# Optimization experiments

Hardware: AMD Instinct MI355X
Metric: run time of the kernel (lower is better)

Reference implementation:

```python
import jax, jax.numpy as jnp
import numpy as np
import math

B, M, C, H = 4, 2048, 512, 8
DQK = C // 4 // H  # 16 per-head query/key dim


def setup_inputs() -> dict:
    key = jax.random.key(0)
    ks = jax.random.split(key, 8)
    s = 0.02
    return {
        "x": jax.random.normal(ks[0], (B, M, C), dtype=jnp.float32),
        "mask": jax.random.randint(ks[1], (B, M), 0, 2, dtype=jnp.int32),
        "Wq": jax.random.normal(ks[2], (C, C // 4), dtype=jnp.float32) * s,
        "bq": jnp.zeros((C // 4,), dtype=jnp.float32),
        "Wk": jax.random.normal(ks[3], (C, C // 4), dtype=jnp.float32) * s,
        "bk": jnp.zeros((C // 4,), dtype=jnp.float32),
        "Wv": jax.random.normal(ks[4], (C, C), dtype=jnp.float32) * s,
        "bv": jnp.zeros((C,), dtype=jnp.float32),
        "gamma": jnp.ones((1,), dtype=jnp.float32),
    }


def reference(x, mask, Wq, bq, Wk, bk, Wv, bv, gamma):
    b, m, c = x.shape
    # projections, split heads: q/k -> (B, H, M, DQK), v -> (B, H, M, C//H)
    q = (x @ Wq + bq).reshape(b, m, H, -1).transpose(0, 2, 1, 3)
    k = (x @ Wk + bk).reshape(b, m, H, -1).transpose(0, 2, 1, 3)
    v = (x @ Wv + bv).reshape(b, m, H, -1).transpose(0, 2, 1, 3)
    scale = 1.0 / math.sqrt(q.shape[-1])
    scores = jnp.einsum('bhmd,bhnd->bhmn', q, k) * scale
    beta = jax.nn.softmax(jax.nn.relu(scores), axis=-1)  # act='relu' pre-softmax
    # att_drop = 0.0 -> identity
    mf = mask.astype(x.dtype)[:, None, None, :]  # (B,1,1,M)
    beta = beta * mf
    beta = beta / (beta.sum(-1, keepdims=True) + 1e-12)
    o = gamma * jnp.einsum('bhmn,bhnd->bhmd', beta, v)  # (B,H,M,C//H)
    return o.transpose(0, 2, 1, 3).reshape(b, m, c)
```

## Files before the change

kernel.cpp:

```cpp
#include <hip/hip_runtime.h>
#include <hip/hip_bf16.h>

#define MSEQ 2048

typedef __attribute__((ext_vector_type(8))) short short8;
typedef __attribute__((ext_vector_type(4))) short short4v;
typedef __attribute__((ext_vector_type(4))) float f32x4;

static __device__ __forceinline__ short bf16b(float f) {
    __hip_bfloat16 h = __float2bfloat16(f);
    return *reinterpret_cast<short*>(&h);
}

static __device__ __forceinline__ void gl_lds16(const void* g, void* l) {
    __builtin_amdgcn_global_load_lds(
        (const __attribute__((address_space(1))) unsigned int*)g,
        (__attribute__((address_space(3))) unsigned int*)l, 16, 0, 0);
}

__global__ __launch_bounds__(256) void xcvt_kernel(
    const float* __restrict__ x, unsigned short* __restrict__ xb)
{
    const size_t i = ((size_t)blockIdx.x * 256 + threadIdx.x) * 8;
    const float4 a = *(const float4*)(x + i);
    const float4 b = *(const float4*)(x + i + 4);
    short8 o;
    o[0]=bf16b(a.x); o[1]=bf16b(a.y); o[2]=bf16b(a.z); o[3]=bf16b(a.w);
    o[4]=bf16b(b.x); o[5]=bf16b(b.y); o[6]=bf16b(b.z); o[7]=bf16b(b.w);
    *(short8*)(xb + i) = o;
}

__global__ __launch_bounds__(256) void wtrans_kernel(
    const float* __restrict__ Wq, const float* __restrict__ Wk,
    const float* __restrict__ Wv, unsigned short* __restrict__ WT)
{
    const int nt = blockIdx.x;
    const int kt = blockIdx.y;
    const int t  = threadIdx.x;
    const int k0 = kt*64;

    const float* W; int ld, n0;
    if (nt < 2)      { W = Wq; ld = 128; n0 = nt*64; }
    else if (nt < 4) { W = Wk; ld = 128; n0 = (nt-2)*64; }
    else             { W = Wv; ld = 512; n0 = (nt-4)*64; }

    __shared__ unsigned short Ts[64*72];

    #pragma unroll
    for (int s = 0; s < 4; ++s) {
        const int lin = s*256 + t;
        const int krow = lin >> 4, ng = lin & 15;
        const float4 v = *(const float4*)(W + (size_t)(k0+krow)*ld + n0 + ng*4);
        Ts[(ng*4+0)*72 + krow] = (unsigned short)bf16b(v.x);
        Ts[(ng*4+1)*72 + krow] = (unsigned short)bf16b(v.y);
        Ts[(ng*4+2)*72 + krow] = (unsigned short)bf16b(v.z);
        Ts[(ng*4+3)*72 + krow] = (unsigned short)bf16b(v.w);
    }
    __syncthreads();
    #pragma unroll
    for (int s = 0; s < 2; ++s) {
        const int lin = s*256 + t;
        const int nrow = lin >> 3, kg = lin & 7;
        *(short8*)(WT + (size_t)(nt*64 + nrow)*512 + k0 + kg*8) = *(const short8*)&Ts[nrow*72 + kg*8];
    }
}

__global__ __launch_bounds__(256, 2) void proj_mfma(
    const unsigned short* __restrict__ xb, const unsigned short* __restrict__ WT,
    const float* __restrict__ bq, const float* __restrict__ bk, const float* __restrict__ bv,
    unsigned short* __restrict__ Qb, unsigned short* __restrict__ Kb, unsigned short* __restrict__ Vt)
{
    const int nt = blockIdx.x;
    const int r0 = blockIdx.y * 128;
    const int n0 = nt * 128;
    const int t = threadIdx.x, w = t >> 6, lane = t & 63, l15 = lane & 15, quad = lane >> 4;
    const int qh = w >> 1, chh = w & 1;

    __shared__ short smem[128*136];
    short* As = smem;
    short* Bs = smem + 128*32;

    f32x4 acc[4][4];
    #pragma unroll
    for (int i = 0; i < 4; ++i)
        #pragma unroll
        for (int j = 0; j < 4; ++j) acc[i][j] = {0.f,0.f,0.f,0.f};

    const int arow = lane >> 2, akg = lane & 3;

    for (int kk = 0; kk < 512; kk += 32) {
        #pragma unroll
        for (int s = 0; s < 2; ++s) {
            const int row = w*32 + s*16 + arow;
            gl_lds16(xb + (size_t)(r0+row)*512 + kk + akg*8, As + (w*32 + s*16)*32);
            gl_lds16(WT + (size_t)(n0+row)*512 + kk + akg*8, Bs + (w*32 + s*16)*32);
        }
        __syncthreads();
        short8 Af[4], Bf[4];
        #pragma unroll
        for (int i = 0; i < 4; ++i) Af[i] = *(const short8*)&As[(qh*64 + i*16 + l15)*32 + quad*8];
        #pragma unroll
        for (int j = 0; j < 4; ++j) Bf[j] = *(const short8*)&Bs[(chh*64 + j*16 + l15)*32 + quad*8];
        #pragma unroll
        for (int i = 0; i < 4; ++i)
            #pragma unroll
            for (int j = 0; j < 4; ++j)
                acc[i][j] = __builtin_amdgcn_mfma_f32_16x16x32_bf16(Af[i], Bf[j], acc[i][j], 0, 0, 0);
        __syncthreads();
    }

    const float* bias = (nt == 0) ? bq : (nt == 1) ? bk : (bv + (nt-2)*128);
    float bj[4];
    #pragma unroll
    for (int j = 0; j < 4; ++j) bj[j] = bias[chh*64 + j*16 + l15];

    short* Ts = smem;
    if (nt < 2) {
        #pragma unroll
        for (int i = 0; i < 4; ++i)
            #pragma unroll
            for (int j = 0; j < 4; ++j)
                #pragma unroll
                for (int r = 0; r < 4; ++r)
                    Ts[(qh*64 + i*16 + quad*4 + r)*136 + chh*64 + j*16 + l15] =
                        bf16b(acc[i][j][r] + bj[j]);
    } else {
        #pragma unroll
        for (int i = 0; i < 4; ++i)
            #pragma unroll
            for (int j = 0; j < 4; ++j)
                #pragma unroll
                for (int r = 0; r < 4; ++r)
                    Ts[(chh*64 + j*16 + l15)*136 + qh*64 + i*16 + quad*4 + r] =
                        bf16b(acc[i][j][r] + bj[j]);
    }
    __syncthreads();

    if (nt < 2) {
        unsigned short* Out = (nt == 0) ? Qb : Kb;
        #pragma unroll
        for (int s = 0; s < 8; ++s) {
            const int lin = s*256 + t, row = lin >> 4, seg = lin & 15;
            *(short8*)(Out + (size_t)(r0+row)*128 + seg*8) = *(const short8*)&Ts[row*136 + seg*8];
        }
    } else {
        const int b = r0 >> 11, key0 = r0 & 2047, chBase = (nt-2)*128;
        #pragma unroll
        for (int s = 0; s < 8; ++s) {
            const int lin = s*256 + t, row = lin >> 4, seg = lin & 15;
            *(short8*)(Vt + ((size_t)(b*512 + chBase + row))*MSEQ + key0 + seg*8) =
                *(const short8*)&Ts[row*136 + seg*8];
        }
    }
}

__global__ __launch_bounds__(256, 4) void attn_mfma(
    const unsigned short* __restrict__ Qb, const unsigned short* __restrict__ Kb,
    const unsigned short* __restrict__ Vt, const int* __restrict__ mask,
    const float* __restrict__ gamma, float* __restrict__ out)
{
    const int bh = blockIdx.x;
    const int b  = bh >> 3, h = bh & 7;
    const int m0 = blockIdx.y * 64;
    const int t  = threadIdx.x;
    const int wave = t >> 6, lane = t & 63, l15 = lane & 15, quad = lane >> 4;

    __shared__ short Ks[64*24];
    __shared__ short Qs[64*24];
    __shared__ short VtS[64*72];
    __shared__ short Ws[64*72];
    __shared__ float msk[64];
    __shared__ float wsl[4*64];
    __shared__ float wsums[64];

    if (t < 64) {
        short8 z = {0,0,0,0,0,0,0,0};
        *(short8*)&Ks[t*24 + 16] = z;
        *(short8*)&Qs[t*24 + 16] = z;
    }
    if (t < 128) {
        const int row = t >> 1, half = t & 1;
        *(short8*)&Qs[row*24 + half*8] =
            *(const short8*)(Qb + (size_t)(b*MSEQ + m0 + row)*128 + h*16 + half*8);
    }
    __syncthreads();

    const int kso = (quad < 2) ? quad*8 : 16;
    short8 qfrag[4];
    #pragma unroll
    for (int c = 0; c < 4; ++c)
        qfrag[c] = *(const short8*)&Qs[(c*16 + l15)*24 + kso];

    f32x4 acc[2][2] = {{{0.f,0.f,0.f,0.f},{0.f,0.f,0.f,0.f}},
                       {{0.f,0.f,0.f,0.f},{0.f,0.f,0.f,0.f}}};
    float wsum_acc[4] = {0.f,0.f,0.f,0.f};
    const int qh = wave >> 1, chh = wave & 1;

    for (int kt = 0; kt < 32; ++kt) {
        const int kn0 = kt*64;
        if (t < 128) {
            const int key = t >> 1, half = t & 1;
            *(short8*)&Ks[key*24 + half*8] =
                *(const short8*)(Kb + (size_t)(b*MSEQ + kn0 + key)*128 + h*16 + half*8);
        }
        #pragma unroll
        for (int i = 0; i < 2; ++i) {
            const int idx = i*256 + t;
            const int kg = idx & 7, ch = idx >> 3;
            *(short8*)&VtS[ch*72 + kg*8] =
                *(const short8*)(Vt + ((size_t)(b*512 + h*64 + ch))*MSEQ + kn0 + kg*8);
        }
        if (t < 64) msk[t] = (float)mask[b*MSEQ + kn0 + t];
        __syncthreads();

        const short8 kfrag = *(const short8*)&Ks[(wave*16 + l15)*24 + kso];
        const float4 mk4 = *(const float4*)&msk[wave*16 + quad*4];
        #pragma unroll
        for (int c = 0; c < 4; ++c) {
            f32x4 s = {0.f,0.f,0.f,0.f};
            s = __builtin_amdgcn_mfma_f32_16x16x32_bf16(kfrag, qfrag[c], s, 0, 0, 0);
            float w0 = mk4.x * __expf(fmaxf(0.25f*s[0], 0.f));
            float w1 = mk4.y * __expf(fmaxf(0.25f*s[1], 0.f));
            float w2 = mk4.z * __expf(fmaxf(0.25f*s[2], 0.f));
            float w3 = mk4.w * __expf(fmaxf(0.25f*s[3], 0.f));
            short4v ws4;
            ws4[0]=bf16b(w0); ws4[1]=bf16b(w1); ws4[2]=bf16b(w2); ws4[3]=bf16b(w3);
            *(short4v*)&Ws[(c*16 + l15)*72 + wave*16 + quad*4] = ws4;
            float tsum = (w0 + w1) + (w2 + w3);
            tsum += __shfl_xor(tsum, 16, 64);
            tsum += __shfl_xor(tsum, 32, 64);
            wsum_acc[c] += tsum;
        }
        __syncthreads();

        short8 Af[2][2], Bf[2][2];
        #pragma unroll
        for (int si = 0; si < 2; ++si)
            #pragma unroll
            for (int kh = 0; kh < 2; ++kh)
                Af[si][kh] = *(const short8*)&Ws[((qh*2+si)*16 + l15)*72 + kh*32 + quad*8];
        #pragma unroll
        for (int ci = 0; ci < 2; ++ci)
            #pragma unroll
            for (int kh = 0; kh < 2; ++kh)
                Bf[ci][kh] = *(const short8*)&VtS[((chh*2+ci)*16 + l15)*72 + kh*32 + quad*8];
        #pragma unroll
        for (int si = 0; si < 2; ++si)
            #pragma unroll
            for (int ci = 0; ci < 2; ++ci)
                #pragma unroll
                for (int kh = 0; kh < 2; ++kh)
                    acc[si][ci] = __builtin_amdgcn_mfma_f32_16x16x32_bf16(
                        Af[si][kh], Bf[ci][kh], acc[si][ci], 0, 0, 0);
        __syncthreads();
    }

    if (quad == 0) {
        #pragma unroll
        for (int c = 0; c < 4; ++c) wsl[wave*64 + c*16 + l15] = wsum_acc[c];
    }
    __syncthreads();
    if (t < 64) wsums[t] = (wsl[t] + wsl[64+t]) + (wsl[128+t] + wsl[192+t]);
    __syncthreads();

    const float g = gamma[0];
    #pragma unroll
    for (int si = 0; si < 2; ++si) {
        #pragma unroll
        for (int r = 0; r < 4; ++r) {
            const int row = qh*32 + si*16 + quad*4 + r;
            const float inv = g / fmaxf(wsums[row], 1e-20f);
            #pragma unroll
            for (int ci = 0; ci < 2; ++ci) {
                const int col = chh*32 + ci*16 + l15;
                out[(size_t)(b*MSEQ + m0 + row)*512 + h*64 + col] = acc[si][ci][r] * inv;
            }
        }
    }
}

extern "C" void kernel_launch(void* const* d_in, const int* in_sizes, int n_in,
                              void* d_out, int out_size, void* d_ws, size_t ws_size,
                              hipStream_t stream) {
    const float* x     = (const float*)d_in[0];
    const int*   mask  = (const int*)  d_in[1];
    const float* Wq    = (const float*)d_in[2];
    const float* bq    = (const float*)d_in[3];
    const float* Wk    = (const float*)d_in[4];
    const float* bk    = (const float*)d_in[5];
    const float* Wv    = (const float*)d_in[6];
    const float* bv    = (const float*)d_in[7];
    const float* gamma = (const float*)d_in[8];
    float* outp = (float*)d_out;

    unsigned short* xb = (unsigned short*)d_ws;
    unsigned short* WT = xb + (size_t)8192*512;
    unsigned short* Qb = WT + (size_t)768*512;
    unsigned short* Kb = Qb + (size_t)8192*128;
    unsigned short* Vt = Kb + (size_t)8192*128;

    xcvt_kernel<<<2048, 256, 0, stream>>>(x, xb);
    wtrans_kernel<<<dim3(12, 8), 256, 0, stream>>>(Wq, Wk, Wv, WT);
    proj_mfma<<<dim3(6, 64), 256, 0, stream>>>(xb, WT, bq, bk, bv, Qb, Kb, Vt);
    attn_mfma<<<dim3(32, 32), 256, 0, stream>>>(Qb, Kb, Vt, mask, gamma, outp);
}
```

Baseline: 168.2 us.

## Halve attention query tile, fold log2e scale into K, use raw exp2

The attention kernel now processes 32 query rows per block instead of 64, doubling the grid and raising the occupancy hint to 8 blocks per CU. The softmax scale times log2(e) is folded into the K projection output, so the inner loop can use a raw v_exp_f32 without a multiply. The per-iteration cross-lane row-sum shuffles are deferred to a single reduction after the loop. In exchange, K and V tiles are reloaded twice as often across blocks, and the scale is now applied before the bf16 rounding of K, which slightly changes precision.

Result: no change. 167.1 us (-0.7%).

```diff
diff --git a/kernel.cpp b/kernel.cpp
--- a/kernel.cpp
+++ b/kernel.cpp
@@ -10,6 +10,12 @@
 static __device__ __forceinline__ short bf16b(float f) {
     __hip_bfloat16 h = __float2bfloat16(f);
     return *reinterpret_cast<short*>(&h);
+}
+
+static __device__ __forceinline__ float fast_exp2(float x) {
+    float r;
+    asm("v_exp_f32 %0, %1" : "=v"(r) : "v"(x));
+    return r;
 }
 
 static __device__ __forceinline__ void gl_lds16(const void* g, void* l) {
@@ -110,6 +116,7 @@
     }
 
     const float* bias = (nt == 0) ? bq : (nt == 1) ? bk : (bv + (nt-2)*128);
+    const float kscale = (nt == 1) ? 0.36067376022224085f : 1.0f;
     float bj[4];
     #pragma unroll
     for (int j = 0; j < 4; ++j) bj[j] = bias[chh*64 + j*16 + l15];
@@ -123,7 +130,7 @@
                 #pragma unroll
                 for (int r = 0; r < 4; ++r)
                     Ts[(qh*64 + i*16 + quad*4 + r)*136 + chh*64 + j*16 + l15] =
-                        bf16b(acc[i][j][r] + bj[j]);
+                        bf16b((acc[i][j][r] + bj[j]) * kscale);
     } else {
         #pragma unroll
         for (int i = 0; i < 4; ++i)
@@ -154,31 +161,31 @@
     }
 }
 
-__global__ __launch_bounds__(256, 4) void attn_mfma(
+__global__ __launch_bounds__(256, 8) void attn_mfma(
     const unsigned short* __restrict__ Qb, const unsigned short* __restrict__ Kb,
     const unsigned short* __restrict__ Vt, const int* __restrict__ mask,
     const float* __restrict__ gamma, float* __restrict__ out)
 {
     const int bh = blockIdx.x;
     const int b  = bh >> 3, h = bh & 7;
-    const int m0 = blockIdx.y * 64;
+    const int m0 = blockIdx.y * 32;
     const int t  = threadIdx.x;
     const int wave = t >> 6, lane = t & 63, l15 = lane & 15, quad = lane >> 4;
 
     __shared__ short Ks[64*24];
-    __shared__ short Qs[64*24];
+    __shared__ short Qs[32*24];
     __shared__ short VtS[64*72];
-    __shared__ short Ws[64*72];
+    __shared__ short Ws[32*72];
     __shared__ float msk[64];
-    __shared__ float wsl[4*64];
-    __shared__ float wsums[64];
-
+    __shared__ float wsl[4*32];
+    __shared__ float wsums[32];
+
+    {
+        short8 z = {0,0,0,0,0,0,0,0};
+        if (t < 64) *(short8*)&Ks[t*24 + 16] = z;
+        if (t < 32) *(short8*)&Qs[t*24 + 16] = z;
+    }
     if (t < 64) {
-        short8 z = {0,0,0,0,0,0,0,0};
-        *(short8*)&Ks[t*24 + 16] = z;
-        *(short8*)&Qs[t*24 + 16] = z;
-    }
-    if (t < 128) {
         const int row = t >> 1, half = t & 1;
         *(short8*)&Qs[row*24 + half*8] =
             *(const short8*)(Qb + (size_t)(b*MSEQ + m0 + row)*128 + h*16 + half*8);
@@ -186,14 +193,13 @@
     __syncthreads();
 
     const int kso = (quad < 2) ? quad*8 : 16;
-    short8 qfrag[4];
-    #pragma unroll
-    for (int c = 0; c < 4; ++c)
+    short8 qfrag[2];
+    #pragma unroll
+    for (int c = 0; c < 2; ++c)
         qfrag[c] = *(const short8*)&Qs[(c*16 + l15)*24 + kso];
 
-    f32x4 acc[2][2] = {{{0.f,0.f,0.f,0.f},{0.f,0.f,0.f,0.f}},
-                       {{0.f,0.f,0.f,0.f},{0.f,0.f,0.f,0.f}}};
-    float wsum_acc[4] = {0.f,0.f,0.f,0.f};
+    f32x4 acc[2] = {{0.f,0.f,0.f,0.f},{0.f,0.f,0.f,0.f}};
+    float wsum_acc[2] = {0.f,0.f};
     const int qh = wave >> 1, chh = wave & 1;
 
     for (int kt = 0; kt < 32; ++kt) {
@@ -216,65 +222,58 @@
         const short8 kfrag = *(const short8*)&Ks[(wave*16 + l15)*24 + kso];
         const float4 mk4 = *(const float4*)&msk[wave*16 + quad*4];
         #pragma unroll
-        for (int c = 0; c < 4; ++c) {
+        for (int c = 0; c < 2; ++c) {
             f32x4 s = {0.f,0.f,0.f,0.f};
             s = __builtin_amdgcn_mfma_f32_16x16x32_bf16(kfrag, qfrag[c], s, 0, 0, 0);
-            float w0 = mk4.x * __expf(fmaxf(0.25f*s[0], 0.f));
-            float w1 = mk4.y * __expf(fmaxf(0.25f*s[1], 0.f));
-            float w2 = mk4.z * __expf(fmaxf(0.25f*s[2], 0.f));
-            float w3 = mk4.w * __expf(fmaxf(0.25f*s[3], 0.f));
+            float w0 = mk4.x * fast_exp2(fmaxf(s[0], 0.f));
+            float w1 = mk4.y * fast_exp2(fmaxf(s[1], 0.f));
+            float w2 = mk4.z * fast_exp2(fmaxf(s[2], 0.f));
+            float w3 = mk4.w * fast_exp2(fmaxf(s[3], 0.f));
             short4v ws4;
             ws4[0]=bf16b(w0); ws4[1]=bf16b(w1); ws4[2]=bf16b(w2); ws4[3]=bf16b(w3);
             *(short4v*)&Ws[(c*16 + l15)*72 + wave*16 + quad*4] = ws4;
-            float tsum = (w0 + w1) + (w2 + w3);
-            tsum += __shfl_xor(tsum, 16, 64);
-            tsum += __shfl_xor(tsum, 32, 64);
-            wsum_acc[c] += tsum;
-        }
-        __syncthreads();
-
-        short8 Af[2][2], Bf[2][2];
-        #pragma unroll
-        for (int si = 0; si < 2; ++si)
-            #pragma unroll
-            for (int kh = 0; kh < 2; ++kh)
-                Af[si][kh] = *(const short8*)&Ws[((qh*2+si)*16 + l15)*72 + kh*32 + quad*8];
+            wsum_acc[c] += (w0 + w1) + (w2 + w3);
+        }
+        __syncthreads();
+
+        short8 Af[2], Bf[2][2];
+        #pragma unroll
+        for (int kh = 0; kh < 2; ++kh)
+            Af[kh] = *(const short8*)&Ws[(qh*16 + l15)*72 + kh*32 + quad*8];
         #pragma unroll
         for (int ci = 0; ci < 2; ++ci)
             #pragma unroll
             for (int kh = 0; kh < 2; ++kh)
                 Bf[ci][kh] = *(const short8*)&VtS[((chh*2+ci)*16 + l15)*72 + kh*32 + quad*8];
         #pragma unroll
-        for (int si = 0; si < 2; ++si)
-            #pragma unroll
-            for (int ci = 0; ci < 2; ++ci)
-                #pragma unroll
-                for (int kh = 0; kh < 2; ++kh)
-                    acc[si][ci] = __builtin_amdgcn_mfma_f32_16x16x32_bf16(
-                        Af[si][kh], Bf[ci][kh], acc[si][ci], 0, 0, 0);
-        __syncthreads();
-    }
-
-    if (quad == 0) {
-        #pragma unroll
-        for (int c = 0; c < 4; ++c) wsl[wave*64 + c*16 + l15] = wsum_acc[c];
-    }
-    __syncthreads();
-    if (t < 64) wsums[t] = (wsl[t] + wsl[64+t]) + (wsl[128+t] + wsl[192+t]);
+        for (int ci = 0; ci < 2; ++ci)
+            #pragma unroll
+            for (int kh = 0; kh < 2; ++kh)
+                acc[ci] = __builtin_amdgcn_mfma_f32_16x16x32_bf16(
+                    Af[kh], Bf[ci][kh], acc[ci], 0, 0, 0);
+        __syncthreads();
+    }
+
+    #pragma unroll
+    for (int c = 0; c < 2; ++c) {
+        float r = wsum_acc[c];
+        r += __shfl_xor(r, 16, 64);
+        r += __shfl_xor(r, 32, 64);
+        if (quad == 0) wsl[wave*32 + c*16 + l15] = r;
+    }
+    __syncthreads();
+    if (t < 32) wsums[t] = (wsl[t] + wsl[32+t]) + (wsl[64+t] + wsl[96+t]);
     __syncthreads();
 
     const float g = gamma[0];
     #pragma unroll
-    for (int si = 0; si < 2; ++si) {
-        #pragma unroll
-        for (int r = 0; r < 4; ++r) {
-            const int row = qh*32 + si*16 + quad*4 + r;
-            const float inv = g / fmaxf(wsums[row], 1e-20f);
-            #pragma unroll
-            for (int ci = 0; ci < 2; ++ci) {
-                const int col = chh*32 + ci*16 + l15;
-                out[(size_t)(b*MSEQ + m0 + row)*512 + h*64 + col] = acc[si][ci][r] * inv;
-            }
+    for (int r = 0; r < 4; ++r) {
+        const int row = qh*16 + quad*4 + r;
+        const float inv = g / fmaxf(wsums[row], 1e-20f);
+        #pragma unroll
+        for (int ci = 0; ci < 2; ++ci) {
+            const int col = chh*32 + ci*16 + l15;
+            out[(size_t)(b*MSEQ + m0 + row)*512 + h*64 + col] = acc[ci][r] * inv;
         }
     }
 }
@@ -302,5 +301,5 @@
     xcvt_kernel<<<2048, 256, 0, stream>>>(x, xb);
     wtrans_kernel<<<dim3(12, 8), 256, 0, stream>>>(Wq, Wk, Wv, WT);
     proj_mfma<<<dim3(6, 64), 256, 0, stream>>>(xb, WT, bq, bk, bv, Qb, Kb, Vt);
-    attn_mfma<<<dim3(32, 32), 256, 0, stream>>>(Qb, Kb, Vt, mask, gamma, outp);
-}
+    attn_mfma<<<dim3(32, 64), 256, 0, stream>>>(Qb, Kb, Vt, mask, gamma, outp);
+}
```

## Split keys across waves in attention kernel, drop LDS staging, fold scale into K

Applied to the files above, without the earlier changes.

The attention kernel now gives each wave a quarter of the key sequence. Each wave loads K, V and mask fragments straight from global memory into registers and uses 16x16x16 bf16 MFMAs that keep P in registers, so the per-tile LDS round trip and the two barriers per key tile go away. The 1/sqrt(d)*log2(e) factor is folded into K during the projection, so the softmax uses a raw v_exp_f32 (exp2). The cost is a final cross-wave reduction of the output accumulators through LDS. Global loads are now uncoalesced, small and not shared across waves, and each thread holds more accumulator registers.

New measurement: 187.9 us. 11.7% more time.

```diff
diff --git a/kernel.cpp b/kernel.cpp
--- a/kernel.cpp
+++ b/kernel.cpp
@@ -10,6 +10,16 @@
 static __device__ __forceinline__ short bf16b(float f) {
     __hip_bfloat16 h = __float2bfloat16(f);
     return *reinterpret_cast<short*>(&h);
+}
+
+static __device__ __forceinline__ float fast_exp2(float x) {
+    float r;
+    asm("v_exp_f32 %0, %1" : "=v"(r) : "v"(x));
+    return r;
+}
+
+static __device__ __forceinline__ f32x4 mfma16(short4v a, short4v b, f32x4 c) {
+    return __builtin_amdgcn_mfma_f32_16x16x16bf16_1k(a, b, c, 0, 0, 0);
 }
 
 static __device__ __forceinline__ void gl_lds16(const void* g, void* l) {
@@ -110,6 +120,7 @@
     }
 
     const float* bias = (nt == 0) ? bq : (nt == 1) ? bk : (bv + (nt-2)*128);
+    const float kscale = (nt == 1) ? 0.36067376022224085f : 1.0f;
     float bj[4];
     #pragma unroll
     for (int j = 0; j < 4; ++j) bj[j] = bias[chh*64 + j*16 + l15];
@@ -123,7 +134,7 @@
                 #pragma unroll
                 for (int r = 0; r < 4; ++r)
                     Ts[(qh*64 + i*16 + quad*4 + r)*136 + chh*64 + j*16 + l15] =
-                        bf16b(acc[i][j][r] + bj[j]);
+                        bf16b((acc[i][j][r] + bj[j]) * kscale);
     } else {
         #pragma unroll
         for (int i = 0; i < 4; ++i)
@@ -163,119 +174,101 @@
     const int b  = bh >> 3, h = bh & 7;
     const int m0 = blockIdx.y * 64;
     const int t  = threadIdx.x;
-    const int wave = t >> 6, lane = t & 63, l15 = lane & 15, quad = lane >> 4;
-
-    __shared__ short Ks[64*24];
-    __shared__ short Qs[64*24];
-    __shared__ short VtS[64*72];
-    __shared__ short Ws[64*72];
-    __shared__ float msk[64];
+    const int w = t >> 6, lane = t & 63, l15 = lane & 15, quad = lane >> 4;
+
+    short4v qf[4];
+    #pragma unroll
+    for (int c = 0; c < 4; ++c)
+        qf[c] = *(const short4v*)(Qb + (size_t)(b*MSEQ + m0 + c*16 + l15)*128 + h*16 + quad*4);
+
+    f32x4 O[4][4];
+    #pragma unroll
+    for (int c = 0; c < 4; ++c)
+        #pragma unroll
+        for (int v = 0; v < 4; ++v) O[c][v] = {0.f,0.f,0.f,0.f};
+    float ws_acc[4] = {0.f,0.f,0.f,0.f};
+
+    const unsigned short* Kp = Kb + (size_t)(b*MSEQ + w*512 + l15)*128 + h*16 + quad*4;
+    const unsigned short* Vp = Vt + ((size_t)(b*512 + h*64 + l15))*MSEQ + w*512 + quad*4;
+    const int* mp = mask + b*MSEQ + w*512 + quad*4;
+
+    #pragma unroll 2
+    for (int s = 0; s < 32; ++s) {
+        const int kn = s*16;
+        const short4v kf = *(const short4v*)(Kp + (size_t)kn*128);
+        const int4 mk = *(const int4*)(mp + kn);
+        short4v vf[4];
+        #pragma unroll
+        for (int v = 0; v < 4; ++v)
+            vf[v] = *(const short4v*)(Vp + (size_t)v*16*MSEQ + kn);
+
+        #pragma unroll
+        for (int c = 0; c < 4; ++c) {
+            f32x4 sc = {0.f,0.f,0.f,0.f};
+            sc = mfma16(kf, qf[c], sc);
+            const float w0 = mk.x ? fast_exp2(fmaxf(sc[0], 0.f)) : 0.f;
+            const float w1 = mk.y ? fast_exp2(fmaxf(sc[1], 0.f)) : 0.f;
+            const float w2 = mk.z ? fast_exp2(fmaxf(sc[2], 0.f)) : 0.f;
+            const float w3 = mk.w ? fast_exp2(fmaxf(sc[3], 0.f)) : 0.f;
+            ws_acc[c] += (w0 + w1) + (w2 + w3);
+            short4v pf;
+            pf[0]=bf16b(w0); pf[1]=bf16b(w1); pf[2]=bf16b(w2); pf[3]=bf16b(w3);
+            #pragma unroll
+            for (int v = 0; v < 4; ++v)
+                O[c][v] = mfma16(pf, vf[v], O[c][v]);
+        }
+    }
+
+    __shared__ float OsA[64*68];
+    __shared__ float OsB[64*68];
     __shared__ float wsl[4*64];
     __shared__ float wsums[64];
 
-    if (t < 64) {
-        short8 z = {0,0,0,0,0,0,0,0};
-        *(short8*)&Ks[t*24 + 16] = z;
-        *(short8*)&Qs[t*24 + 16] = z;
-    }
-    if (t < 128) {
-        const int row = t >> 1, half = t & 1;
-        *(short8*)&Qs[row*24 + half*8] =
-            *(const short8*)(Qb + (size_t)(b*MSEQ + m0 + row)*128 + h*16 + half*8);
-    }
-    __syncthreads();
-
-    const int kso = (quad < 2) ? quad*8 : 16;
-    short8 qfrag[4];
-    #pragma unroll
-    for (int c = 0; c < 4; ++c)
-        qfrag[c] = *(const short8*)&Qs[(c*16 + l15)*24 + kso];
-
-    f32x4 acc[2][2] = {{{0.f,0.f,0.f,0.f},{0.f,0.f,0.f,0.f}},
-                       {{0.f,0.f,0.f,0.f},{0.f,0.f,0.f,0.f}}};
-    float wsum_acc[4] = {0.f,0.f,0.f,0.f};
-    const int qh = wave >> 1, chh = wave & 1;
-
-    for (int kt = 0; kt < 32; ++kt) {
-        const int kn0 = kt*64;
-        if (t < 128) {
-            const int key = t >> 1, half = t & 1;
-            *(short8*)&Ks[key*24 + half*8] =
-                *(const short8*)(Kb + (size_t)(b*MSEQ + kn0 + key)*128 + h*16 + half*8);
-        }
-        #pragma unroll
-        for (int i = 0; i < 2; ++i) {
-            const int idx = i*256 + t;
-            const int kg = idx & 7, ch = idx >> 3;
-            *(short8*)&VtS[ch*72 + kg*8] =
-                *(const short8*)(Vt + ((size_t)(b*512 + h*64 + ch))*MSEQ + kn0 + kg*8);
-        }
-        if (t < 64) msk[t] = (float)mask[b*MSEQ + kn0 + t];
-        __syncthreads();
-
-        const short8 kfrag = *(const short8*)&Ks[(wave*16 + l15)*24 + kso];
-        const float4 mk4 = *(const float4*)&msk[wave*16 + quad*4];
-        #pragma unroll
-        for (int c = 0; c < 4; ++c) {
-            f32x4 s = {0.f,0.f,0.f,0.f};
-            s = __builtin_amdgcn_mfma_f32_16x16x32_bf16(kfrag, qfrag[c], s, 0, 0, 0);
-            float w0 = mk4.x * __expf(fmaxf(0.25f*s[0], 0.f));
-            float w1 = mk4.y * __expf(fmaxf(0.25f*s[1], 0.f));
-            float w2 = mk4.z * __expf(fmaxf(0.25f*s[2], 0.f));
-            float w3 = mk4.w * __expf(fmaxf(0.25f*s[3], 0.f));
-            short4v ws4;
-            ws4[0]=bf16b(w0); ws4[1]=bf16b(w1); ws4[2]=bf16b(w2); ws4[3]=bf16b(w3);
-            *(short4v*)&Ws[(c*16 + l15)*72 + wave*16 + quad*4] = ws4;
-            float tsum = (w0 + w1) + (w2 + w3);
-            tsum += __shfl_xor(tsum, 16, 64);
-            tsum += __shfl_xor(tsum, 32, 64);
-            wsum_acc[c] += tsum;
-        }
-        __syncthreads();
-
-        short8 Af[2][2], Bf[2][2];
-        #pragma unroll
-        for (int si = 0; si < 2; ++si)
-            #pragma unroll
-            for (int kh = 0; kh < 2; ++kh)
-                Af[si][kh] = *(const short8*)&Ws[((qh*2+si)*16 + l15)*72 + kh*32 + quad*8];
-        #pragma unroll
-        for (int ci = 0; ci < 2; ++ci)
-            #pragma unroll
-            for (int kh = 0; kh < 2; ++kh)
-                Bf[ci][kh] = *(const short8*)&VtS[((chh*2+ci)*16 + l15)*72 + kh*32 + quad*8];
-        #pragma unroll
-        for (int si = 0; si < 2; ++si)
-            #pragma unroll
-            for (int ci = 0; ci < 2; ++ci)
-                #pragma unroll
-                for (int kh = 0; kh < 2; ++kh)
-                    acc[si][ci] = __builtin_amdgcn_mfma_f32_16x16x32_bf16(
-                        Af[si][kh], Bf[ci][kh], acc[si][ci], 0, 0, 0);
-        __syncthreads();
-    }
-
-    if (quad == 0) {
-        #pragma unroll
-        for (int c = 0; c < 4; ++c) wsl[wave*64 + c*16 + l15] = wsum_acc[c];
-    }
-    __syncthreads();
+    #pragma unroll
+    for (int c = 0; c < 4; ++c) {
+        float r = ws_acc[c];
+        r += __shfl_xor(r, 16, 64);
+        r += __shfl_xor(r, 32, 64);
+        if (quad == 0) wsl[w*64 + c*16 + l15] = r;
+    }
+
+    if (w == 0 || w == 2) {
+        float* buf = (w == 2) ? OsB : OsA;
+        #pragma unroll
+        for (int c = 0; c < 4; ++c)
+            #pragma unroll
+            for (int v = 0; v < 4; ++v)
+                #pragma unroll
+                for (int r = 0; r < 4; ++r)
+                    buf[(c*16 + quad*4 + r)*68 + v*16 + l15] = O[c][v][r];
+    }
+    __syncthreads();
+    if (w == 1 || w == 3) {
+        float* buf = (w == 3) ? OsB : OsA;
+        #pragma unroll
+        for (int c = 0; c < 4; ++c)
+            #pragma unroll
+            for (int v = 0; v < 4; ++v)
+                #pragma unroll
+                for (int r = 0; r < 4; ++r)
+                    buf[(c*16 + quad*4 + r)*68 + v*16 + l15] += O[c][v][r];
+    }
     if (t < 64) wsums[t] = (wsl[t] + wsl[64+t]) + (wsl[128+t] + wsl[192+t]);
     __syncthreads();
 
     const float g = gamma[0];
     #pragma unroll
-    for (int si = 0; si < 2; ++si) {
-        #pragma unroll
-        for (int r = 0; r < 4; ++r) {
-            const int row = qh*32 + si*16 + quad*4 + r;
-            const float inv = g / fmaxf(wsums[row], 1e-20f);
-            #pragma unroll
-            for (int ci = 0; ci < 2; ++ci) {
-                const int col = chh*32 + ci*16 + l15;
-                out[(size_t)(b*MSEQ + m0 + row)*512 + h*64 + col] = acc[si][ci][r] * inv;
-            }
-        }
+    for (int s2 = 0; s2 < 4; ++s2) {
+        const int lin = s2*256 + t;
+        const int q = lin >> 4, seg = lin & 15;
+        const float inv = g / fmaxf(wsums[q], 1e-20f);
+        const int o = q*68 + seg*4;
+        float4 vv;
+        vv.x = (OsA[o+0] + OsB[o+0]) * inv;
+        vv.y = (OsA[o+1] + OsB[o+1]) * inv;
+        vv.z = (OsA[o+2] + OsB[o+2]) * inv;
+        vv.w = (OsA[o+3] + OsB[o+3]) * inv;
+        *(float4*)(out + (size_t)(b*MSEQ + m0 + q)*512 + h*64 + seg*4) = vv;
     }
 }
 
```
